# Optimization experiments

Measured on AMD Instinct MI355X. Metric: run time of the kernel, lower is better.

## Reference

```python
import jax, jax.numpy as jnp
import numpy as np

BATCH, SEQ, D_MODEL = 2, 4096, 1024
D_STATE, EXPAND = 64, 2
D_INNER = D_MODEL * EXPAND


def setup_inputs() -> dict:
    key = jax.random.key(0)
    ks = jax.random.split(key, 12)
    s = 0.02
    return {
        "x": jax.random.normal(ks[0], (BATCH, SEQ, D_MODEL), dtype=jnp.float32),
        "W_in": jax.random.normal(ks[1], (D_MODEL, 2 * D_INNER), dtype=jnp.float32) * s,
        "b_in": jnp.zeros((2 * D_INNER,), dtype=jnp.float32),
        "W_xp": jax.random.normal(ks[2], (D_INNER, D_STATE), dtype=jnp.float32) * s,
        "b_xp": jnp.zeros((D_STATE,), dtype=jnp.float32),
        "W_dt": jax.random.normal(ks[3], (D_INNER, D_MODEL), dtype=jnp.float32) * s,
        "b_dt": jnp.zeros((D_MODEL,), dtype=jnp.float32),
        "W_out": jax.random.normal(ks[4], (D_INNER, D_MODEL), dtype=jnp.float32) * s,
        "b_out": jnp.zeros((D_MODEL,), dtype=jnp.float32),
        "A_log": jax.random.normal(ks[5], (D_STATE,), dtype=jnp.float32),
        "D": jax.random.normal(ks[6], (D_MODEL,), dtype=jnp.float32),
    }


def _silu(v):
    return v * jax.nn.sigmoid(v)


def reference(x, W_in, b_in, W_xp, b_xp, W_dt, b_dt, W_out, b_out, A_log, D):
    # in_proj -> split into inner stream and residual gate
    xr = x @ W_in + b_in                       # [B,S,2*d_inner]
    x_inner, res = jnp.split(xr, 2, axis=-1)   # each [B,S,d_inner]
    x_inner = _silu(x_inner)

    A = -jnp.exp(A_log)                        # [N]
    delta = jax.nn.softplus(x_inner @ W_dt + b_dt)  # [B,S,d_model]
    mean_delta = delta.mean(axis=-1)           # [B,S] (scalar dt per step, as in source)
    a = jnp.exp(A[None, None, :] * mean_delta[..., None])  # [B,S,N] discrete A
    bx = x_inner @ W_xp + b_xp                 # [B,S,N] input injection

    # sequential selective-scan recurrence: state = a_t * state + bx_t
    def step(state, inp):
        a_t, bx_t = inp                        # [B,N] each
        state = a_t * state + bx_t
        return state, state.sum(axis=-1)       # emit per-batch scalar

    init = jnp.zeros((x.shape[0], D_STATE), dtype=x.dtype)
    _, s_sum = jax.lax.scan(step, init, (a.transpose(1, 0, 2), bx.transpose(1, 0, 2)))
    s_sum = s_sum.T                            # [B,S]

    y = s_sum[..., None] * x_inner             # [B,S,d_inner]
    y = y * _silu(res)
    out = y @ W_out + b_out + x * D
    return out
```

## Files before the change

### kernel.cpp

```cpp
#include <hip/hip_runtime.h>

#define SEQ 4096
#define DMODEL 1024
#define DSTATE 64
#define DINNER 2048
#define MROWS 8192
#define NCAT 1152
#define NCHUNK 64
#define LCHUNK 64

typedef __attribute__((ext_vector_type(8))) __bf16 bf16x8;
typedef __attribute__((ext_vector_type(8))) short short8;
typedef __attribute__((ext_vector_type(4))) float floatx4;

__device__ inline float bf2f(short s) {
  union { unsigned u; float f; } c;
  c.u = ((unsigned)(unsigned short)s) << 16;
  return c.f;
}
__device__ inline short f2bf(float f) {
  union { float f; unsigned u; } c; c.f = f;
  unsigned r = 0x7fffu + ((c.u >> 16) & 1u);
  return (short)((c.u + r) >> 16);
}
__device__ inline float silu_f(float v) {
  return v * __builtin_amdgcn_rcpf(1.f + __expf(-v));
}
__device__ inline float softplus_f(float v) {
  return fmaxf(v, 0.f) + log1pf(__expf(-fabsf(v)));
}
__device__ inline void gld_lds16(const void* g, void* l) {
  __builtin_amdgcn_global_load_lds(
      (__attribute__((address_space(1))) void*)g,
      (__attribute__((address_space(3))) void*)l, 16, 0, 0);
}

__device__ inline size_t permOff(int r, int k, int K) {
  return (((size_t)(r >> 4) * (K >> 3) + (k >> 3)) << 7) + ((r & 15) << 3) + (k & 7);
}

#define PP0 4096
#define PP1 (PP0 + 4096)
#define PP2 (PP1 + 2048)
#define PP3 (PP2 + 128)
#define PP4 (PP3 + 2048)

__device__ void tile_transpose_perm(const float* __restrict__ in, short* __restrict__ out,
                                    int R, int C, int bx, int by, float (*tile)[33]) {
  const int tx = threadIdx.x & 31, ty = threadIdx.x >> 5;
  const int cb = bx * 32, rb = by * 32;
#pragma unroll
  for (int i = 0; i < 32; i += 8) {
    int r = rb + ty + i, c = cb + tx;
    tile[ty + i][tx] = (r < R && c < C) ? in[(size_t)r * C + c] : 0.f;
  }
  __syncthreads();
#pragma unroll
  for (int i = 0; i < 32; i += 8) {
    int orow = cb + ty + i, oc = rb + tx;
    if (orow < C && oc < R) out[permOff(orow, oc, R)] = f2bf(tile[tx][ty + i]);
  }
}

__global__ void prepass_kernel(const float* __restrict__ x, short* __restrict__ x_bf,
                               const float* __restrict__ W_in, short* __restrict__ Wt_in,
                               const float* __restrict__ W_dt, const float* __restrict__ W_xp,
                               short* __restrict__ Bcat,
                               const float* __restrict__ W_out, short* __restrict__ Wt_out) {
  __shared__ float tile[32][33];
  const int blk = blockIdx.x;
  if (blk < PP0) {
    int o = blk * 256 + threadIdx.x;
    int m = o & 15, rest = o >> 4;
    int c = rest & 127, p = rest >> 7;
    const float* src = x + ((size_t)(p * 16 + m)) * 1024 + c * 8;
    float4 v0 = ((const float4*)src)[0];
    float4 v1 = ((const float4*)src)[1];
    short8 ov;
    ov[0] = f2bf(v0.x); ov[1] = f2bf(v0.y); ov[2] = f2bf(v0.z); ov[3] = f2bf(v0.w);
    ov[4] = f2bf(v1.x); ov[5] = f2bf(v1.y); ov[6] = f2bf(v1.z); ov[7] = f2bf(v1.w);
    ((short8*)x_bf)[o] = ov;
  } else if (blk < PP1) {
    int t = blk - PP0;
    tile_transpose_perm(W_in, Wt_in, 1024, 4096, t & 127, t >> 7, tile);
  } else if (blk < PP2) {
    int t = blk - PP1;
    tile_transpose_perm(W_dt, Bcat, 2048, 1024, t & 31, t >> 5, tile);
  } else if (blk < PP3) {
    int t = blk - PP2;
    tile_transpose_perm(W_xp, Bcat + (size_t)1024 * DINNER, 2048, 64, t & 1, t >> 1, tile);
  } else {
    int t = blk - PP3;
    tile_transpose_perm(W_out, Wt_out, 2048, 1024, t & 31, t >> 5, tile);
  }
}

template <int MODE, int KTOT, int KSL, int NB, int Z>
__global__ __launch_bounds__(256) void gemm_bt(
    const short* __restrict__ A, const short* __restrict__ Bt,
    const float* __restrict__ bias,
    void* __restrict__ out0, void* __restrict__ out1)
{
  __shared__ __attribute__((aligned(16))) short sA[128 * 64];
  __shared__ __attribute__((aligned(16))) short sB[128 * 64];

  const int tid = threadIdx.x;
  const int lane = tid & 63;
  const int w = tid >> 6;
  const int wr = w >> 1, wc = w & 1;
  const int m = lane & 15, quad = lane >> 4;

  const int xcd = blockIdx.x & 7;
  const int rest = blockIdx.x >> 3;
  constexpr int PXB = 8 * NB;
  const int z = rest / PXB;
  const int q2 = rest - z * PXB;
  const int bM = (xcd * 8 + (q2 & 7)) * 128;
  const int bN = (q2 >> 3) * 128;
  constexpr int N = NB * 128;

  floatx4 acc[4][4] = {};

  const size_t PS = (size_t)KTOT * 16;
  const short* Apan0 = A  + ((size_t)(bM >> 4) + w) * PS + lane * 8;
  const short* Apan1 = Apan0 + 4 * PS;
  const short* Bpan0 = Bt + ((size_t)(bN >> 4) + w) * PS + lane * 8;
  const short* Bpan1 = Bpan0 + 4 * PS;
  short* dA0 = sA + w * 1024;
  short* dA1 = sA + (w + 4) * 1024;
  short* dB0 = sB + w * 1024;
  short* dB1 = sB + (w + 4) * 1024;

  const int kbeg = z * KSL;
  for (int k0 = kbeg; k0 < kbeg + KSL; k0 += 64) {
    __syncthreads();
    const size_t ko = (size_t)k0 * 16;
    gld_lds16(Apan0 + ko,       dA0);
    gld_lds16(Apan0 + ko + 512, dA0 + 512);
    gld_lds16(Apan1 + ko,       dA1);
    gld_lds16(Apan1 + ko + 512, dA1 + 512);
    gld_lds16(Bpan0 + ko,       dB0);
    gld_lds16(Bpan0 + ko + 512, dB0 + 512);
    gld_lds16(Bpan1 + ko,       dB1);
    gld_lds16(Bpan1 + ko + 512, dB1 + 512);
    __syncthreads();
#pragma unroll
    for (int kh = 0; kh < 2; ++kh) {
      bf16x8 af[4], bf[4];
#pragma unroll
      for (int rt = 0; rt < 4; ++rt)
        af[rt] = *(const bf16x8*)(sA + (wr * 4 + rt) * 1024 + (kh * 4 + quad) * 128 + m * 8);
#pragma unroll
      for (int ct = 0; ct < 4; ++ct)
        bf[ct] = *(const bf16x8*)(sB + (wc * 4 + ct) * 1024 + (kh * 4 + quad) * 128 + m * 8);
#pragma unroll
      for (int rt = 0; rt < 4; ++rt)
#pragma unroll
        for (int ct = 0; ct < 4; ++ct)
          acc[rt][ct] = __builtin_amdgcn_mfma_f32_16x16x32_bf16(af[rt], bf[ct], acc[rt][ct], 0, 0, 0);
    }
  }

  const int rowbase = bM + wr * 64;
  const int colbase = bN + wc * 64;

  if (MODE == 0) {
    short* dst = (bN < DINNER) ? (short*)out0 : (short*)out1;
    const int cb = (bN < DINNER) ? colbase : colbase - DINNER;
#pragma unroll
    for (int rt = 0; rt < 4; ++rt) {
      const size_t rowPan = ((size_t)((rowbase >> 4) + rt)) << 8;
#pragma unroll
      for (int ct = 0; ct < 4; ++ct) {
        const int colA = colbase + ct * 16 + m;
        const int colP = cb + ct * 16 + m;
        const size_t base = ((rowPan + (colP >> 3)) << 7) + (colP & 7) + ((size_t)quad * 32);
#pragma unroll
        for (int reg = 0; reg < 4; ++reg) {
          float val = acc[rt][ct][reg] + bias[colA];
          dst[base + reg * 8] = f2bf(silu_f(val));
        }
      }
    }
  } else {
    if (NB == 9 && colbase >= 1088) return;
    short* dst = (short*)out0 + (size_t)z * MROWS * N;
#pragma unroll
    for (int rt = 0; rt < 4; ++rt)
#pragma unroll
      for (int ct = 0; ct < 4; ++ct) {
        const int col = colbase + ct * 16 + m;
#pragma unroll
        for (int reg = 0; reg < 4; ++reg) {
          const int r = rowbase + rt * 16 + quad * 4 + reg;
          dst[(size_t)r * N + col] = f2bf(acc[rt][ct][reg]);
        }
      }
  }
}

template <int MODE, int KTOT, int KSL, int NT, int ZS>
__global__ __launch_bounds__(512, 2) void gemm256(
    const short* __restrict__ A, const short* __restrict__ Bt,
    const float* __restrict__ bias,
    void* __restrict__ out0, void* __restrict__ out1)
{
  __shared__ __attribute__((aligned(16))) short sLds[65536];

  const int tid = threadIdx.x;
  const int lane = tid & 63;
  const int w = tid >> 6;
  const int wr = w >> 2, wc = w & 3;
  const int m = lane & 15, quad = lane >> 4;

  const int xcd = blockIdx.x & 7;
  const int q = blockIdx.x >> 3;
  const int mt = xcd * 4 + (q & 3);
  const int rest = q >> 2;
  const int ntile = rest % NT;
  const int z = rest / NT;
  const int bM = mt * 256, bN = ntile * 256;
  const int kbeg = z * KSL;

  floatx4 acc[8][4] = {};

  const size_t PS = (size_t)KTOT * 16;
  const short* AgA = A  + ((size_t)(bM >> 4) + w) * PS + (size_t)kbeg * 16 + lane * 8;
  const short* AgB = AgA + 8 * PS;
  const short* BgA = Bt + ((size_t)(bN >> 4) + w) * PS + (size_t)kbeg * 16 + lane * 8;
  const short* BgB = BgA + 8 * PS;

  constexpr int KT = KSL / 64;

  auto STAGE_Q = [&](int t, int qq) {
    const size_t go = (size_t)t * 1024 + (size_t)(qq >> 1) * 512;
    short* d = sLds + ((t & 1) << 15) + ((qq & 1) << 14) + ((qq >> 1) << 13) + w * 512;
    const short* g0 = (qq & 1) ? BgA : AgA;
    const short* g1 = (qq & 1) ? BgB : AgB;
    gld_lds16(g0 + go, d);
    gld_lds16(g1 + go, d + 4096);
  };

  const int aoff = wr * 4096 + quad * 128 + m * 8;
  const int boff = 16384 + wc * 2048 + quad * 128 + m * 8;

  bf16x8 aA[4], aB[4], bA[4], bB[4];

  STAGE_Q(0, 0); STAGE_Q(0, 1); STAGE_Q(0, 2); STAGE_Q(0, 3);
  asm volatile("s_waitcnt vmcnt(4)" ::: "memory");
  asm volatile("s_barrier" ::: "memory");
  {
    const short* bs = sLds;
#pragma unroll
    for (int rt = 0; rt < 4; ++rt) aA[rt] = *(const bf16x8*)(bs + aoff + rt * 512);
#pragma unroll
    for (int ct = 0; ct < 4; ++ct) bA[ct] = *(const bf16x8*)(bs + boff + ct * 512);
    if (KT > 1) STAGE_Q(1, 0);
    __builtin_amdgcn_sched_barrier(0);
  }

#pragma unroll 1
  for (int t = 0; t < KT; ++t) {
    const short* bs = sLds + ((t & 1) << 15);
    const bool pf = (t + 1 < KT);

#pragma unroll
    for (int rt = 0; rt < 4; ++rt) aB[rt] = *(const bf16x8*)(bs + aoff + (4 + rt) * 512);
    if (pf) {
      STAGE_Q(t + 1, 1);
      asm volatile("s_waitcnt vmcnt(4)" ::: "memory");
    } else {
      asm volatile("s_waitcnt vmcnt(0)" ::: "memory");
    }
    __builtin_amdgcn_sched_barrier(0);
    __builtin_amdgcn_s_setprio(1);
#pragma unroll
    for (int rt = 0; rt < 4; ++rt)
#pragma unroll
      for (int ct = 0; ct < 4; ++ct)
        acc[rt][ct] = __builtin_amdgcn_mfma_f32_16x16x32_bf16(aA[rt], bA[ct], acc[rt][ct], 0, 0, 0);
    __builtin_amdgcn_s_setprio(0);
    __builtin_amdgcn_sched_barrier(0);

    asm volatile("s_waitcnt lgkmcnt(0)" ::: "memory");
    asm volatile("s_barrier" ::: "memory");
#pragma unroll
    for (int rt = 0; rt < 4; ++rt) aA[rt] = *(const bf16x8*)(bs + 8192 + aoff + rt * 512);
#pragma unroll
    for (int ct = 0; ct < 4; ++ct) bB[ct] = *(const bf16x8*)(bs + 8192 + boff + ct * 512);
    if (pf) STAGE_Q(t + 1, 2);
    __builtin_amdgcn_sched_barrier(0);
    __builtin_amdgcn_s_setprio(1);
#pragma unroll
    for (int rt = 0; rt < 4; ++rt)
#pragma unroll
      for (int ct = 0; ct < 4; ++ct)
        acc[4 + rt][ct] = __builtin_amdgcn_mfma_f32_16x16x32_bf16(aB[rt], bA[ct], acc[4 + rt][ct], 0, 0, 0);
    __builtin_amdgcn_s_setprio(0);
    __builtin_amdgcn_sched_barrier(0);

#pragma unroll
    for (int rt = 0; rt < 4; ++rt) aB[rt] = *(const bf16x8*)(bs + 8192 + aoff + (4 + rt) * 512);
    if (pf) {
      STAGE_Q(t + 1, 3);
      asm volatile("s_waitcnt vmcnt(4)" ::: "memory");
    }
    __builtin_amdgcn_sched_barrier(0);
    __builtin_amdgcn_s_setprio(1);
#pragma unroll
    for (int rt = 0; rt < 4; ++rt)
#pragma unroll
      for (int ct = 0; ct < 4; ++ct)
        acc[rt][ct] = __builtin_amdgcn_mfma_f32_16x16x32_bf16(aA[rt], bB[ct], acc[rt][ct], 0, 0, 0);
    __builtin_amdgcn_s_setprio(0);
    __builtin_amdgcn_sched_barrier(0);

    if (pf) {
      asm volatile("s_waitcnt lgkmcnt(0)" ::: "memory");
      asm volatile("s_barrier" ::: "memory");
      const short* bs2 = sLds + (((t + 1) & 1) << 15);
#pragma unroll
      for (int rt = 0; rt < 4; ++rt) aA[rt] = *(const bf16x8*)(bs2 + aoff + rt * 512);
#pragma unroll
      for (int ct = 0; ct < 4; ++ct) bA[ct] = *(const bf16x8*)(bs2 + boff + ct * 512);
      if (t + 2 < KT) STAGE_Q(t + 2, 0);
      __builtin_amdgcn_sched_barrier(0);
    }
    __builtin_amdgcn_s_setprio(1);
#pragma unroll
    for (int rt = 0; rt < 4; ++rt)
#pragma unroll
      for (int ct = 0; ct < 4; ++ct)
        acc[4 + rt][ct] = __builtin_amdgcn_mfma_f32_16x16x32_bf16(aB[rt], bB[ct], acc[4 + rt][ct], 0, 0, 0);
    __builtin_amdgcn_s_setprio(0);
    __builtin_amdgcn_sched_barrier(0);
  }

  const int rowbase = bM + wr * 128;
  const int colbase = bN + wc * 64;

  if constexpr (MODE == 0) {
    short* dst = (bN < DINNER) ? (short*)out0 : (short*)out1;
    const int cb = (bN < DINNER) ? colbase : colbase - DINNER;
#pragma unroll
    for (int rt = 0; rt < 8; ++rt) {
      const size_t rowPan = ((size_t)(rowbase >> 4) + rt) << 8;
#pragma unroll
      for (int ct = 0; ct < 4; ++ct) {
        const int colA = colbase + ct * 16 + m;
        const int colP = cb + ct * 16 + m;
        const size_t base = ((rowPan + (colP >> 3)) << 7) + (colP & 7) + ((size_t)quad * 32);
        const float bv = bias[colA];
#pragma unroll
        for (int reg = 0; reg < 4; ++reg) {
          float val = acc[rt][ct][reg] + bv;
          dst[base + reg * 8] = f2bf(silu_f(val));
        }
      }
    }
  } else {
    constexpr int N = NT * 256;
    short* dst = (short*)out0 + (size_t)z * MROWS * N;
#pragma unroll
    for (int rt = 0; rt < 8; ++rt)
#pragma unroll
      for (int ct = 0; ct < 4; ++ct) {
        const int col = colbase + ct * 16 + m;
#pragma unroll
        for (int reg = 0; reg < 4; ++reg) {
          const int r = rowbase + rt * 16 + quad * 4 + reg;
          dst[(size_t)r * N + col] = f2bf(acc[rt][ct][reg]);
        }
      }
  }
}

__global__ void g2_epilogue(const short* __restrict__ p, const float* __restrict__ b_dt,
                            const float* __restrict__ b_xp,
                            float* __restrict__ md_sum, float* __restrict__ bx) {
  const int row = blockIdx.x * 4 + (threadIdx.x >> 6);
  const int lane = threadIdx.x & 63;
  const size_t base0 = (size_t)row * NCAT;
  const size_t base1 = base0 + (size_t)MROWS * NCAT;
  short8 a0 = *(const short8*)(p + base0 + lane * 16);
  short8 a1 = *(const short8*)(p + base0 + lane * 16 + 8);
  short8 c0 = *(const short8*)(p + base1 + lane * 16);
  short8 c1 = *(const short8*)(p + base1 + lane * 16 + 8);
  float s = 0.f;
#pragma unroll
  for (int j = 0; j < 8; ++j) {
    s += softplus_f(bf2f(a0[j]) + bf2f(c0[j]) + b_dt[lane * 16 + j]);
    s += softplus_f(bf2f(a1[j]) + bf2f(c1[j]) + b_dt[lane * 16 + 8 + j]);
  }
  s += __shfl_xor(s, 1);  s += __shfl_xor(s, 2);  s += __shfl_xor(s, 4);
  s += __shfl_xor(s, 8);  s += __shfl_xor(s, 16); s += __shfl_xor(s, 32);
  if (lane == 0) md_sum[row] = s;
  bx[(size_t)row * DSTATE + lane] =
      bf2f(p[base0 + 1024 + lane]) + bf2f(p[base1 + 1024 + lane]) + b_xp[lane];
}

__global__ void g4_epilogue(const short* __restrict__ p, const float* __restrict__ b_out,
                            const float* __restrict__ x, const float* __restrict__ Dv,
                            float* __restrict__ out) {
  const int r = blockIdx.x, c = threadIdx.x * 4;
  const size_t o = (size_t)r * DMODEL + c;
  short4 a0 = *(const short4*)(p + o);
  short4 a1 = *(const short4*)(p + (size_t)MROWS * DMODEL + o);
  float4 xv = *(const float4*)(x + o);
  float4 ov;
  ov.x = bf2f(a0.x) + bf2f(a1.x) + b_out[c + 0] + xv.x * Dv[c + 0];
  ov.y = bf2f(a0.y) + bf2f(a1.y) + b_out[c + 1] + xv.y * Dv[c + 1];
  ov.z = bf2f(a0.z) + bf2f(a1.z) + b_out[c + 2] + xv.z * Dv[c + 2];
  ov.w = bf2f(a0.w) + bf2f(a1.w) + b_out[c + 3] + xv.w * Dv[c + 3];
  *(float4*)(out + o) = ov;
}

__global__ void scan_phase1(const float* __restrict__ md_sum, const float* __restrict__ A_log,
                            const float* __restrict__ bx,
                            float* __restrict__ chunk_prod, float* __restrict__ chunk_end) {
  const int n = threadIdx.x;
  const int c = blockIdx.x & (NCHUNK - 1);
  const int b = blockIdx.x >> 6;
  const float An = -__expf(A_log[n]);
  float prod = 1.f, st = 0.f;
  const int t0 = c * LCHUNK;
#pragma unroll 4
  for (int i = 0; i < LCHUNK; ++i) {
    const int t = t0 + i;
    const float md = md_sum[b * SEQ + t] * (1.f / DMODEL);
    const float a = __expf(An * md);
    st = a * st + bx[((size_t)(b * SEQ + t)) * DSTATE + n];
    prod *= a;
  }
  chunk_prod[(b * NCHUNK + c) * DSTATE + n] = prod;
  chunk_end [(b * NCHUNK + c) * DSTATE + n] = st;
}

__global__ void scan_phase3(const float* __restrict__ md_sum, const float* __restrict__ A_log,
                            const float* __restrict__ bx,
                            const float* __restrict__ chunk_prod,
                            const float* __restrict__ chunk_end,
                            float* __restrict__ s_sum) {
  const int n = threadIdx.x;
  const int c = blockIdx.x & (NCHUNK - 1);
  const int b = blockIdx.x >> 6;
  const float An = -__expf(A_log[n]);
  float st = 0.f;
  for (int cc = 0; cc < c; ++cc) {
    const size_t idx = ((size_t)(b * NCHUNK + cc)) * DSTATE + n;
    st = chunk_prod[idx] * st + chunk_end[idx];
  }
  const int t0 = c * LCHUNK;
#pragma unroll 4
  for (int i = 0; i < LCHUNK; ++i) {
    const int t = t0 + i;
    const float md = md_sum[b * SEQ + t] * (1.f / DMODEL);
    const float a = __expf(An * md);
    st = a * st + bx[((size_t)(b * SEQ + t)) * DSTATE + n];
    float v = st;
    v += __shfl_xor(v, 32); v += __shfl_xor(v, 16); v += __shfl_xor(v, 8);
    v += __shfl_xor(v, 4);  v += __shfl_xor(v, 2);  v += __shfl_xor(v, 1);
    if (n == 0) s_sum[b * SEQ + t] = v;
  }
}

__global__ void ymul_kernel(const short* __restrict__ xi, const short* __restrict__ g,
                            const float* __restrict__ s_sum, short* __restrict__ y) {
  const int o = blockIdx.x * 256 + threadIdx.x;
  const int row = ((o >> 12) << 4) | (o & 15);
  const size_t base = (size_t)o * 8;
  const float s = s_sum[row];
  short8 xv = *(const short8*)(xi + base);
  short8 gv = *(const short8*)(g + base);
  short8 yv;
#pragma unroll
  for (int k = 0; k < 8; ++k) yv[k] = f2bf(s * bf2f(xv[k]) * bf2f(gv[k]));
  *(short8*)(y + base) = yv;
}

extern "C" void kernel_launch(void* const* d_in, const int* in_sizes, int n_in,
                              void* d_out, int out_size, void* d_ws, size_t ws_size,
                              hipStream_t stream) {
  const float* x     = (const float*)d_in[0];
  const float* W_in  = (const float*)d_in[1];
  const float* b_in  = (const float*)d_in[2];
  const float* W_xp  = (const float*)d_in[3];
  const float* b_xp  = (const float*)d_in[4];
  const float* W_dt  = (const float*)d_in[5];
  const float* b_dt  = (const float*)d_in[6];
  const float* W_out = (const float*)d_in[7];
  const float* b_out = (const float*)d_in[8];
  const float* A_log = (const float*)d_in[9];
  const float* Dv    = (const float*)d_in[10];

  char* ws = (char*)d_ws;
  size_t off = 0;
  auto alloc = [&](size_t bytes) -> void* {
    void* p = (void*)(ws + off);
    off += (bytes + 255) & ~(size_t)255;
    return p;
  };
  short* x_bf    = (short*)alloc((size_t)MROWS * DMODEL * 2);
  short* Wt_in   = (short*)alloc((size_t)4096 * 1024 * 2);
  short* Bcat    = (short*)alloc((size_t)NCAT * DINNER * 2);
  short* Wt_out  = (short*)alloc((size_t)1024 * 2048 * 2);
  short* xi      = (short*)alloc((size_t)MROWS * DINNER * 2);
  short* gbuf    = (short*)alloc((size_t)MROWS * DINNER * 2);
  short* ybuf    = (short*)alloc((size_t)MROWS * DINNER * 2);
  short* p2      = (short*)alloc((size_t)2 * MROWS * NCAT * 2);
  float* md_sum  = (float*)alloc((size_t)MROWS * 4);
  float* bx      = (float*)alloc((size_t)MROWS * DSTATE * 4);
  float* cprod   = (float*)alloc((size_t)2 * NCHUNK * DSTATE * 4);
  float* cend    = (float*)alloc((size_t)2 * NCHUNK * DSTATE * 4);
  float* s_sum   = (float*)alloc((size_t)MROWS * 4);

  prepass_kernel<<<PP4, 256, 0, stream>>>(x, x_bf, W_in, Wt_in, W_dt, W_xp, Bcat, W_out, Wt_out);

  gemm256<0, 1024, 1024, 16, 1><<<512, 512, 0, stream>>>(x_bf, Wt_in, b_in, xi, gbuf);
  gemm_bt<1, 2048, 1024, 9, 2><<<1152, 256, 0, stream>>>(xi, Bcat, nullptr, p2, nullptr);
  g2_epilogue<<<MROWS / 4, 256, 0, stream>>>(p2, b_dt, b_xp, md_sum, bx);
  scan_phase1<<<2 * NCHUNK, DSTATE, 0, stream>>>(md_sum, A_log, bx, cprod, cend);
  scan_phase3<<<2 * NCHUNK, DSTATE, 0, stream>>>(md_sum, A_log, bx, cprod, cend, s_sum);
  ymul_kernel<<<MROWS * DINNER / 8 / 256, 256, 0, stream>>>(xi, gbuf, s_sum, ybuf);
  gemm256<1, 2048, 1024, 4, 2><<<256, 512, 0, stream>>>(ybuf, Wt_out, nullptr, xi, nullptr);
  g4_epilogue<<<MROWS, 256, 0, stream>>>(xi, b_out, x, Dv, (float*)d_out);
}
```

Before: 389.5 us.

## Split dt/xp GEMM: use 256-tile GEMM for dt, dedicated small GEMM for xp

The combined dt+xp projection (N=1152, with the last 128-wide tile half wasted) previously ran through a 128x128-tile kernel. It now runs the 1024-wide dt projection through the larger 256-tile gemm256 kernel, plus a separate double-buffered xp_gemm kernel that computes the 64-wide xp projection as split-K fp32 partials. The split-K xp partials and bias are summed inside the scan kernels instead of in the epilogue. This trades padded-tile waste and a less efficient GEMM for one extra kernel launch and extra fp32 reads in the scan.

```diff
diff --git a/kernel.cpp b/kernel.cpp
--- a/kernel.cpp
+++ b/kernel.cpp
@@ -95,110 +95,6 @@
   }
 }
 
-template <int MODE, int KTOT, int KSL, int NB, int Z>
-__global__ __launch_bounds__(256) void gemm_bt(
-    const short* __restrict__ A, const short* __restrict__ Bt,
-    const float* __restrict__ bias,
-    void* __restrict__ out0, void* __restrict__ out1)
-{
-  __shared__ __attribute__((aligned(16))) short sA[128 * 64];
-  __shared__ __attribute__((aligned(16))) short sB[128 * 64];
-
-  const int tid = threadIdx.x;
-  const int lane = tid & 63;
-  const int w = tid >> 6;
-  const int wr = w >> 1, wc = w & 1;
-  const int m = lane & 15, quad = lane >> 4;
-
-  const int xcd = blockIdx.x & 7;
-  const int rest = blockIdx.x >> 3;
-  constexpr int PXB = 8 * NB;
-  const int z = rest / PXB;
-  const int q2 = rest - z * PXB;
-  const int bM = (xcd * 8 + (q2 & 7)) * 128;
-  const int bN = (q2 >> 3) * 128;
-  constexpr int N = NB * 128;
-
-  floatx4 acc[4][4] = {};
-
-  const size_t PS = (size_t)KTOT * 16;
-  const short* Apan0 = A  + ((size_t)(bM >> 4) + w) * PS + lane * 8;
-  const short* Apan1 = Apan0 + 4 * PS;
-  const short* Bpan0 = Bt + ((size_t)(bN >> 4) + w) * PS + lane * 8;
-  const short* Bpan1 = Bpan0 + 4 * PS;
-  short* dA0 = sA + w * 1024;
-  short* dA1 = sA + (w + 4) * 1024;
-  short* dB0 = sB + w * 1024;
-  short* dB1 = sB + (w + 4) * 1024;
-
-  const int kbeg = z * KSL;
-  for (int k0 = kbeg; k0 < kbeg + KSL; k0 += 64) {
-    __syncthreads();
-    const size_t ko = (size_t)k0 * 16;
-    gld_lds16(Apan0 + ko,       dA0);
-    gld_lds16(Apan0 + ko + 512, dA0 + 512);
-    gld_lds16(Apan1 + ko,       dA1);
-    gld_lds16(Apan1 + ko + 512, dA1 + 512);
-    gld_lds16(Bpan0 + ko,       dB0);
-    gld_lds16(Bpan0 + ko + 512, dB0 + 512);
-    gld_lds16(Bpan1 + ko,       dB1);
-    gld_lds16(Bpan1 + ko + 512, dB1 + 512);
-    __syncthreads();
-#pragma unroll
-    for (int kh = 0; kh < 2; ++kh) {
-      bf16x8 af[4], bf[4];
-#pragma unroll
-      for (int rt = 0; rt < 4; ++rt)
-        af[rt] = *(const bf16x8*)(sA + (wr * 4 + rt) * 1024 + (kh * 4 + quad) * 128 + m * 8);
-#pragma unroll
-      for (int ct = 0; ct < 4; ++ct)
-        bf[ct] = *(const bf16x8*)(sB + (wc * 4 + ct) * 1024 + (kh * 4 + quad) * 128 + m * 8);
-#pragma unroll
-      for (int rt = 0; rt < 4; ++rt)
-#pragma unroll
-        for (int ct = 0; ct < 4; ++ct)
-          acc[rt][ct] = __builtin_amdgcn_mfma_f32_16x16x32_bf16(af[rt], bf[ct], acc[rt][ct], 0, 0, 0);
-    }
-  }
-
-  const int rowbase = bM + wr * 64;
-  const int colbase = bN + wc * 64;
-
-  if (MODE == 0) {
-    short* dst = (bN < DINNER) ? (short*)out0 : (short*)out1;
-    const int cb = (bN < DINNER) ? colbase : colbase - DINNER;
-#pragma unroll
-    for (int rt = 0; rt < 4; ++rt) {
-      const size_t rowPan = ((size_t)((rowbase >> 4) + rt)) << 8;
-#pragma unroll
-      for (int ct = 0; ct < 4; ++ct) {
-        const int colA = colbase + ct * 16 + m;
-        const int colP = cb + ct * 16 + m;
-        const size_t base = ((rowPan + (colP >> 3)) << 7) + (colP & 7) + ((size_t)quad * 32);
-#pragma unroll
-        for (int reg = 0; reg < 4; ++reg) {
-          float val = acc[rt][ct][reg] + bias[colA];
-          dst[base + reg * 8] = f2bf(silu_f(val));
-        }
-      }
-    }
-  } else {
-    if (NB == 9 && colbase >= 1088) return;
-    short* dst = (short*)out0 + (size_t)z * MROWS * N;
-#pragma unroll
-    for (int rt = 0; rt < 4; ++rt)
-#pragma unroll
-      for (int ct = 0; ct < 4; ++ct) {
-        const int col = colbase + ct * 16 + m;
-#pragma unroll
-        for (int reg = 0; reg < 4; ++reg) {
-          const int r = rowbase + rt * 16 + quad * 4 + reg;
-          dst[(size_t)r * N + col] = f2bf(acc[rt][ct][reg]);
-        }
-      }
-  }
-}
-
 template <int MODE, int KTOT, int KSL, int NT, int ZS>
 __global__ __launch_bounds__(512, 2) void gemm256(
     const short* __restrict__ A, const short* __restrict__ Bt,
@@ -375,13 +271,63 @@
   }
 }
 
+__global__ __launch_bounds__(256) void xp_gemm(const short* __restrict__ xi,
+                                               const short* __restrict__ Bxp,
+                                               float* __restrict__ bxp) {
+  __shared__ __attribute__((aligned(16))) short sA[2][4096];
+  __shared__ __attribute__((aligned(16))) short sB[2][4096];
+  const int tid = threadIdx.x, lane = tid & 63, w = tid >> 6;
+  const int m = lane & 15, quad = lane >> 4;
+  const int z = blockIdx.x >> 7;
+  const int rb = (blockIdx.x & 127) * 64;
+  const size_t PS = (size_t)2048 * 16;
+  const short* Ag = xi  + ((size_t)(rb >> 4) + w) * PS + (size_t)z * 1024 * 16 + lane * 8;
+  const short* Bg = Bxp + (size_t)w * PS + (size_t)z * 1024 * 16 + lane * 8;
+  floatx4 acc[4] = {};
+  auto STAGE = [&](int t) {
+    const size_t go = (size_t)t * 1024;
+    short* da = sA[t & 1] + w * 1024;
+    short* db = sB[t & 1] + w * 1024;
+    gld_lds16(Ag + go, da); gld_lds16(Ag + go + 512, da + 512);
+    gld_lds16(Bg + go, db); gld_lds16(Bg + go + 512, db + 512);
+  };
+  STAGE(0);
+#pragma unroll 1
+  for (int t = 0; t < 16; ++t) {
+    __builtin_amdgcn_s_barrier();
+    if (t + 1 < 16) {
+      STAGE(t + 1);
+      asm volatile("s_waitcnt vmcnt(4)" ::: "memory");
+    } else {
+      asm volatile("s_waitcnt vmcnt(0)" ::: "memory");
+    }
+    __builtin_amdgcn_s_barrier();
+    const short* a0 = sA[t & 1] + w * 1024 + quad * 128 + m * 8;
+    const short* b0 = sB[t & 1] + quad * 128 + m * 8;
+#pragma unroll
+    for (int kh = 0; kh < 2; ++kh) {
+      bf16x8 a = *(const bf16x8*)(a0 + kh * 512);
+#pragma unroll
+      for (int ct = 0; ct < 4; ++ct) {
+        bf16x8 b = *(const bf16x8*)(b0 + ct * 1024 + kh * 512);
+        acc[ct] = __builtin_amdgcn_mfma_f32_16x16x32_bf16(a, b, acc[ct], 0, 0, 0);
+      }
+    }
+  }
+  float* dst = bxp + (size_t)z * MROWS * DSTATE;
+#pragma unroll
+  for (int ct = 0; ct < 4; ++ct)
+#pragma unroll
+    for (int reg = 0; reg < 4; ++reg)
+      dst[(size_t)(rb + w * 16 + quad * 4 + reg) * DSTATE + ct * 16 + m] = acc[ct][reg];
+}
+
 __global__ void g2_epilogue(const short* __restrict__ p, const float* __restrict__ b_dt,
-                            const float* __restrict__ b_xp,
-                            float* __restrict__ md_sum, float* __restrict__ bx) {
+                            float* __restrict__ md_sum) {
   const int row = blockIdx.x * 4 + (threadIdx.x >> 6);
   const int lane = threadIdx.x & 63;
-  const size_t base0 = (size_t)row * NCAT;
-  const size_t base1 = base0 + (size_t)MROWS * NCAT;
+  const size_t base0 = (size_t)row * 1024;
+  const size_t base1 = base0 + (size_t)MROWS * 1024;
   short8 a0 = *(const short8*)(p + base0 + lane * 16);
   short8 a1 = *(const short8*)(p + base0 + lane * 16 + 8);
   short8 c0 = *(const short8*)(p + base1 + lane * 16);
@@ -395,8 +341,6 @@
   s += __shfl_xor(s, 1);  s += __shfl_xor(s, 2);  s += __shfl_xor(s, 4);
   s += __shfl_xor(s, 8);  s += __shfl_xor(s, 16); s += __shfl_xor(s, 32);
   if (lane == 0) md_sum[row] = s;
-  bx[(size_t)row * DSTATE + lane] =
-      bf2f(p[base0 + 1024 + lane]) + bf2f(p[base1 + 1024 + lane]) + b_xp[lane];
 }
 
 __global__ void g4_epilogue(const short* __restrict__ p, const float* __restrict__ b_out,
@@ -416,12 +360,15 @@
 }
 
 __global__ void scan_phase1(const float* __restrict__ md_sum, const float* __restrict__ A_log,
-                            const float* __restrict__ bx,
+                            const float* __restrict__ bxp, const float* __restrict__ b_xp,
                             float* __restrict__ chunk_prod, float* __restrict__ chunk_end) {
   const int n = threadIdx.x;
   const int c = blockIdx.x & (NCHUNK - 1);
   const int b = blockIdx.x >> 6;
   const float An = -__expf(A_log[n]);
+  const float bxn = b_xp[n];
+  const float* bx0 = bxp;
+  const float* bx1 = bxp + (size_t)MROWS * DSTATE;
   float prod = 1.f, st = 0.f;
   const int t0 = c * LCHUNK;
 #pragma unroll 4
@@ -429,7 +376,8 @@
     const int t = t0 + i;
     const float md = md_sum[b * SEQ + t] * (1.f / DMODEL);
     const float a = __expf(An * md);
-    st = a * st + bx[((size_t)(b * SEQ + t)) * DSTATE + n];
+    const size_t idx = ((size_t)(b * SEQ + t)) * DSTATE + n;
+    st = a * st + (bx0[idx] + bx1[idx] + bxn);
     prod *= a;
   }
   chunk_prod[(b * NCHUNK + c) * DSTATE + n] = prod;
@@ -437,7 +385,7 @@
 }
 
 __global__ void scan_phase3(const float* __restrict__ md_sum, const float* __restrict__ A_log,
-                            const float* __restrict__ bx,
+                            const float* __restrict__ bxp, const float* __restrict__ b_xp,
                             const float* __restrict__ chunk_prod,
                             const float* __restrict__ chunk_end,
                             float* __restrict__ s_sum) {
@@ -445,7 +393,11 @@
   const int c = blockIdx.x & (NCHUNK - 1);
   const int b = blockIdx.x >> 6;
   const float An = -__expf(A_log[n]);
+  const float bxn = b_xp[n];
+  const float* bx0 = bxp;
+  const float* bx1 = bxp + (size_t)MROWS * DSTATE;
   float st = 0.f;
+#pragma unroll 4
   for (int cc = 0; cc < c; ++cc) {
     const size_t idx = ((size_t)(b * NCHUNK + cc)) * DSTATE + n;
     st = chunk_prod[idx] * st + chunk_end[idx];
@@ -456,7 +408,8 @@
     const int t = t0 + i;
     const float md = md_sum[b * SEQ + t] * (1.f / DMODEL);
     const float a = __expf(An * md);
-    st = a * st + bx[((size_t)(b * SEQ + t)) * DSTATE + n];
+    const size_t idx = ((size_t)(b * SEQ + t)) * DSTATE + n;
+    st = a * st + (bx0[idx] + bx1[idx] + bxn);
     float v = st;
     v += __shfl_xor(v, 32); v += __shfl_xor(v, 16); v += __shfl_xor(v, 8);
     v += __shfl_xor(v, 4);  v += __shfl_xor(v, 2);  v += __shfl_xor(v, 1);
@@ -507,9 +460,9 @@
   short* xi      = (short*)alloc((size_t)MROWS * DINNER * 2);
   short* gbuf    = (short*)alloc((size_t)MROWS * DINNER * 2);
   short* ybuf    = (short*)alloc((size_t)MROWS * DINNER * 2);
-  short* p2      = (short*)alloc((size_t)2 * MROWS * NCAT * 2);
+  short* p2      = (short*)alloc((size_t)2 * MROWS * 1024 * 2);
   float* md_sum  = (float*)alloc((size_t)MROWS * 4);
-  float* bx      = (float*)alloc((size_t)MROWS * DSTATE * 4);
+  float* bxp     = (float*)alloc((size_t)2 * MROWS * DSTATE * 4);
   float* cprod   = (float*)alloc((size_t)2 * NCHUNK * DSTATE * 4);
   float* cend    = (float*)alloc((size_t)2 * NCHUNK * DSTATE * 4);
   float* s_sum   = (float*)alloc((size_t)MROWS * 4);
@@ -517,10 +470,11 @@
   prepass_kernel<<<PP4, 256, 0, stream>>>(x, x_bf, W_in, Wt_in, W_dt, W_xp, Bcat, W_out, Wt_out);
 
   gemm256<0, 1024, 1024, 16, 1><<<512, 512, 0, stream>>>(x_bf, Wt_in, b_in, xi, gbuf);
-  gemm_bt<1, 2048, 1024, 9, 2><<<1152, 256, 0, stream>>>(xi, Bcat, nullptr, p2, nullptr);
-  g2_epilogue<<<MROWS / 4, 256, 0, stream>>>(p2, b_dt, b_xp, md_sum, bx);
-  scan_phase1<<<2 * NCHUNK, DSTATE, 0, stream>>>(md_sum, A_log, bx, cprod, cend);
-  scan_phase3<<<2 * NCHUNK, DSTATE, 0, stream>>>(md_sum, A_log, bx, cprod, cend, s_sum);
+  gemm256<1, 2048, 1024, 4, 2><<<256, 512, 0, stream>>>(xi, Bcat, nullptr, p2, nullptr);
+  xp_gemm<<<256, 256, 0, stream>>>(xi, Bcat + (size_t)1024 * DINNER, bxp);
+  g2_epilogue<<<MROWS / 4, 256, 0, stream>>>(p2, b_dt, md_sum);
+  scan_phase1<<<2 * NCHUNK, DSTATE, 0, stream>>>(md_sum, A_log, bxp, b_xp, cprod, cend);
+  scan_phase3<<<2 * NCHUNK, DSTATE, 0, stream>>>(md_sum, A_log, bxp, b_xp, cprod, cend, s_sum);
   ymul_kernel<<<MROWS * DINNER / 8 / 256, 256, 0, stream>>>(xi, gbuf, s_sum, ybuf);
   gemm256<1, 2048, 1024, 4, 2><<<256, 512, 0, stream>>>(ybuf, Wt_out, nullptr, xi, nullptr);
   g4_epilogue<<<MROWS, 256, 0, stream>>>(xi, b_out, x, Dv, (float*)d_out);
```

New measurement: 376.1 us. 3.4% less time.
